# Kernel optimization log

Measured on AMD Instinct MI355X. Metric: run time of the kernel, lower is better.

Reference implementation:

```python
import jax, jax.numpy as jnp
import numpy as np

MASK_VAL = -2.0**32 + 1.0

def setup_inputs() -> dict:
    key = jax.random.key(0)
    ks = jax.random.split(key, 8)
    B, T, E = 4096, 200, 64
    H1, H2 = 64, 32
    return {
        "query": jax.random.normal(ks[0], (B, 1, E), dtype=jnp.float32),
        "keys": jax.random.normal(ks[1], (B, T, E), dtype=jnp.float32),
        "keys_len": jax.random.randint(ks[2], (B, 1), 0, T, dtype=jnp.int64),
        "W1": jax.random.normal(ks[3], (4 * E, H1), dtype=jnp.float32) * 0.05,
        "b1": jnp.zeros((H1,), dtype=jnp.float32),
        "W2": jax.random.normal(ks[4], (H1, H2), dtype=jnp.float32) * 0.05,
        "b2": jnp.zeros((H2,), dtype=jnp.float32),
        "W3": jax.random.normal(ks[5], (H2, 1), dtype=jnp.float32) * 0.05,
        "b3": jnp.zeros((1,), dtype=jnp.float32),
    }

def reference(query, keys, keys_len, W1, b1, W2, b2, W3, b3):
    B, T, E = keys.shape
    q = jnp.broadcast_to(query, (B, T, E))                      # (B,T,E)
    x = jnp.concatenate([q, keys, q - keys, q * keys], axis=-1)  # (B,T,4E)
    h = jax.nn.relu(jnp.einsum('bti,ih->bth', x, W1) + b1)       # (B,T,H1)
    h = jax.nn.relu(jnp.einsum('bth,ho->bto', h, W2) + b2)       # (B,T,H2)
    score = jnp.einsum('bto,oc->btc', h, W3) + b3                # (B,T,1)
    score = jnp.transpose(score, (0, 2, 1))                      # (B,1,T)
    mask = (jnp.arange(T)[None, :] < keys_len)[:, None, :]       # (B,1,T)
    scores = jnp.where(mask, score, jnp.float32(MASK_VAL))
    scores = jax.nn.softmax(scores, axis=-1)                     # weight_normalization=True
    return jnp.matmul(scores, keys)                              # (B,1,E)
```

## Files before the change

### kernel.cpp

```cpp
#include <hip/hip_runtime.h>

typedef __attribute__((ext_vector_type(8))) short short8_t;
typedef __attribute__((ext_vector_type(4))) float f32x4;

#define MASK_VAL (-4294967295.0f)
#define NEG_BIG  (-1e30f)

__device__ __forceinline__ short f2bf(float x) {
    unsigned u;
    __builtin_memcpy(&u, &x, 4);
    u += 0x7FFFu + ((u >> 16) & 1u);
    return (short)(u >> 16);
}
__device__ __forceinline__ float bf2f(short s) {
    unsigned u = ((unsigned)(unsigned short)s) << 16;
    float f;
    __builtin_memcpy(&f, &u, 4);
    return f;
}

__global__ void prep_fold(const float* __restrict__ W1, const float* __restrict__ W2,
                          void* __restrict__ ws)
{
    short* wkT = (short*)ws;
    short* wdT = wkT + 4096;
    short* w2T = wkT + 8192;
    float* wac = (float*)((char*)ws + 20480);
    const int tid = threadIdx.x;
    for (int idx = tid; idx < 4096; idx += 256) {
        int n = idx & 63, k = idx >> 6;
        float a  = W1[4096  + idx];
        float c  = W1[8192  + idx];
        float d  = W1[12288 + idx];
        wkT[n * 64 + k] = f2bf(a - c);
        wdT[n * 64 + k] = f2bf(d);
        wac[idx] = W1[idx] + c;
    }
    for (int idx = tid; idx < 2048; idx += 256) {
        int o = idx & 31, h = idx >> 5;
        w2T[o * 64 + h] = f2bf(W2[idx]);
    }
}

__global__ __launch_bounds__(256) void prep_cs(
    const float* __restrict__ query, const float* __restrict__ b1,
    void* __restrict__ ws, int B)
{
    const float* wac = (const float*)((const char*)ws + 20480);
    float* csAll     = (float*)((char*)ws + 36864);
    __shared__ float wacs[4096];
    __shared__ float qsb[16 * 64];
    __shared__ float b1s[64];
    const int tid = threadIdx.x;
    const int g0  = blockIdx.x * 16;
    for (int i = tid; i < 1024; i += 256)
        ((float4*)wacs)[i] = ((const float4*)wac)[i];
    {
        int nb = B - g0; if (nb > 16) nb = 16;
        for (int i = tid; i < nb * 16; i += 256)
            ((float4*)qsb)[i] = ((const float4*)(query + (size_t)g0 * 64))[i];
    }
    if (tid < 64) b1s[tid] = b1[tid];
    __syncthreads();
    for (int o = tid; o < 1024; o += 256) {
        int bb = o >> 6, h = o & 63;
        if (g0 + bb >= B) continue;
        float acc = b1s[h];
#pragma unroll 16
        for (int i = 0; i < 64; ++i)
            acc += qsb[bb * 64 + i] * wacs[i * 64 + h];
        csAll[(size_t)(g0 + bb) * 64 + h] = acc;
    }
}

__global__ __launch_bounds__(256, 2) void attn_main(
    const float* __restrict__ query,
    const float* __restrict__ keys,
    const int*   __restrict__ keys_len,
    const float* __restrict__ b2,
    const float* __restrict__ W3,
    const float* __restrict__ b3,
    const void*  __restrict__ ws,
    float* __restrict__ out,
    int B)
{
    constexpr int STR = 72;
    const short* wkT   = (const short*)ws;
    const short* wdT   = wkT + 4096;
    const short* w2T   = wkT + 8192;
    const float* csAll = (const float*)((const char*)ws + 36864);

    __shared__ short Bk[64 * STR];
    __shared__ short Bd[64 * STR];
    __shared__ short W2s[32 * STR];
    __shared__ short h1w[4][16 * STR];
    __shared__ float swv[4][16];

    const int tid  = threadIdx.x;
    const int lane = tid & 63;
    const int wid  = tid >> 6;
    const int col  = lane & 15;
    const int quad = lane >> 4;
    const int b    = blockIdx.x * 4 + wid;
    const bool act = (b < B);

    for (int c = tid; c < 512; c += 256) {
        int r = c >> 3, ch = (c & 7) * 8;
        *(short8_t*)&Bk[r * STR + ch] = *(const short8_t*)(wkT + r * 64 + ch);
        *(short8_t*)&Bd[r * STR + ch] = *(const short8_t*)(wdT + r * 64 + ch);
    }
    {
        int r = tid >> 3, ch = (tid & 7) * 8;
        *(short8_t*)&W2s[r * STR + ch] = *(const short8_t*)(w2T + r * 64 + ch);
    }

    const float* kb = nullptr;
    float4 n0, n1, n2, n3;
    float4 qv0, qv1, qv2, qv3;
    float cs0 = 0.f, cs1 = 0.f, cs2 = 0.f, cs3 = 0.f;
    float b2a = 0.f, b2b = 0.f, w3a = 0.f, w3b = 0.f, b3v = 0.f;
    if (act) {
        kb = keys + (size_t)b * 12800;
        {
            const float* kr = kb + col * 64 + quad * 8;
            n0 = *(const float4*)(kr);
            n1 = *(const float4*)(kr + 4);
            n2 = *(const float4*)(kr + 32);
            n3 = *(const float4*)(kr + 36);
        }
        const float* qb = query + (size_t)b * 64;
        qv0 = *(const float4*)(qb + quad * 8);
        qv1 = *(const float4*)(qb + quad * 8 + 4);
        qv2 = *(const float4*)(qb + 32 + quad * 8);
        qv3 = *(const float4*)(qb + 32 + quad * 8 + 4);
        const float* cb = csAll + (size_t)b * 64;
        cs0 = cb[col]; cs1 = cb[16 + col]; cs2 = cb[32 + col]; cs3 = cb[48 + col];
        b2a = b2[col];      b2b = b2[col + 16];
        w3a = W3[col];      w3b = W3[col + 16];
        b3v = b3[0];
    }
    __syncthreads();
    if (!act) return;

    const int len = keys_len[b];
    short* hw = h1w[wid];

    float m_run = NEG_BIG, l_run = 0.f;
    float accv[16];
#pragma unroll
    for (int i = 0; i < 16; ++i) accv[i] = 0.f;

    for (int jt = 0; jt < 13; ++jt) {
        float4 k0 = n0, k1 = n1, k2 = n2, k3 = n3;
        if (jt < 12) {
            int row = jt * 16 + 16 + col;
            row = row < 200 ? row : 199;
            const float* kr = kb + row * 64 + quad * 8;
            n0 = *(const float4*)(kr);
            n1 = *(const float4*)(kr + 4);
            n2 = *(const float4*)(kr + 32);
            n3 = *(const float4*)(kr + 36);
        }

        short8_t aK0, aK1, aQ0, aQ1;
        aK0[0] = f2bf(k0.x); aK0[1] = f2bf(k0.y); aK0[2] = f2bf(k0.z); aK0[3] = f2bf(k0.w);
        aK0[4] = f2bf(k1.x); aK0[5] = f2bf(k1.y); aK0[6] = f2bf(k1.z); aK0[7] = f2bf(k1.w);
        aK1[0] = f2bf(k2.x); aK1[1] = f2bf(k2.y); aK1[2] = f2bf(k2.z); aK1[3] = f2bf(k2.w);
        aK1[4] = f2bf(k3.x); aK1[5] = f2bf(k3.y); aK1[6] = f2bf(k3.z); aK1[7] = f2bf(k3.w);
        aQ0[0] = f2bf(k0.x * qv0.x); aQ0[1] = f2bf(k0.y * qv0.y);
        aQ0[2] = f2bf(k0.z * qv0.z); aQ0[3] = f2bf(k0.w * qv0.w);
        aQ0[4] = f2bf(k1.x * qv1.x); aQ0[5] = f2bf(k1.y * qv1.y);
        aQ0[6] = f2bf(k1.z * qv1.z); aQ0[7] = f2bf(k1.w * qv1.w);
        aQ1[0] = f2bf(k2.x * qv2.x); aQ1[1] = f2bf(k2.y * qv2.y);
        aQ1[2] = f2bf(k2.z * qv2.z); aQ1[3] = f2bf(k2.w * qv2.w);
        aQ1[4] = f2bf(k3.x * qv3.x); aQ1[5] = f2bf(k3.y * qv3.y);
        aQ1[6] = f2bf(k3.z * qv3.z); aQ1[7] = f2bf(k3.w * qv3.w);

        f32x4 acc[4] = {f32x4{0,0,0,0}, f32x4{0,0,0,0}, f32x4{0,0,0,0}, f32x4{0,0,0,0}};
#pragma unroll
        for (int nt = 0; nt < 4; ++nt) {
            const short* bp = &Bk[(nt * 16 + col) * STR + quad * 8];
            const short* dp = &Bd[(nt * 16 + col) * STR + quad * 8];
            acc[nt] = __builtin_amdgcn_mfma_f32_16x16x32_bf16(aK0, *(const short8_t*)bp,        acc[nt], 0, 0, 0);
            acc[nt] = __builtin_amdgcn_mfma_f32_16x16x32_bf16(aK1, *(const short8_t*)(bp + 32), acc[nt], 0, 0, 0);
            acc[nt] = __builtin_amdgcn_mfma_f32_16x16x32_bf16(aQ0, *(const short8_t*)dp,        acc[nt], 0, 0, 0);
            acc[nt] = __builtin_amdgcn_mfma_f32_16x16x32_bf16(aQ1, *(const short8_t*)(dp + 32), acc[nt], 0, 0, 0);
        }

        float csv[4] = {cs0, cs1, cs2, cs3};
#pragma unroll
        for (int nt = 0; nt < 4; ++nt) {
            float cadd = csv[nt];
#pragma unroll
            for (int r = 0; r < 4; ++r)
                hw[(quad * 4 + r) * STR + nt * 16 + col] = f2bf(fmaxf(acc[nt][r] + cadd, 0.f));
        }

        f32x4 acc2a = f32x4{0,0,0,0}, acc2b = f32x4{0,0,0,0};
#pragma unroll
        for (int ks = 0; ks < 2; ++ks) {
            short8_t a2 = *(const short8_t*)&hw[col * STR + ks * 32 + quad * 8];
            acc2a = __builtin_amdgcn_mfma_f32_16x16x32_bf16(
                a2, *(const short8_t*)&W2s[col * STR + ks * 32 + quad * 8], acc2a, 0, 0, 0);
            acc2b = __builtin_amdgcn_mfma_f32_16x16x32_bf16(
                a2, *(const short8_t*)&W2s[(16 + col) * STR + ks * 32 + quad * 8], acc2b, 0, 0, 0);
        }

#pragma unroll
        for (int r = 0; r < 4; ++r) {
            float v = fmaxf(acc2a[r] + b2a, 0.f) * w3a
                    + fmaxf(acc2b[r] + b2b, 0.f) * w3b;
            v += __shfl_xor(v, 1);
            v += __shfl_xor(v, 2);
            v += __shfl_xor(v, 4);
            v += __shfl_xor(v, 8);
            if (col == 0) swv[wid][quad * 4 + r] = v + b3v;
        }
        float sv = swv[wid][col];

        int  row  = jt * 16 + col;
        bool vrow = row < 200;
        sv = (row < len) ? sv : MASK_VAL;
        float svm = vrow ? sv : NEG_BIG;
        svm = fmaxf(svm, __shfl_xor(svm, 1));
        svm = fmaxf(svm, __shfl_xor(svm, 2));
        svm = fmaxf(svm, __shfl_xor(svm, 4));
        svm = fmaxf(svm, __shfl_xor(svm, 8));
        float m_new = fmaxf(m_run, svm);
        float p = vrow ? __expf(sv - m_new) : 0.f;
        float ps = p;
        ps += __shfl_xor(ps, 1);
        ps += __shfl_xor(ps, 2);
        ps += __shfl_xor(ps, 4);
        ps += __shfl_xor(ps, 8);
        if (m_new > m_run) {
            float scale = __expf(m_run - m_new);
            l_run *= scale;
#pragma unroll
            for (int i = 0; i < 16; ++i) accv[i] *= scale;
            m_run = m_new;
        }
        l_run += ps;
#pragma unroll
        for (int i = 0; i < 8; ++i) {
            accv[i]     += p * bf2f(aK0[i]);
            accv[8 + i] += p * bf2f(aK1[i]);
        }
    }

    float inv = 1.f / l_run;
#pragma unroll
    for (int i = 0; i < 16; ++i) {
        float v = accv[i];
        v += __shfl_xor(v, 1);
        v += __shfl_xor(v, 2);
        v += __shfl_xor(v, 4);
        v += __shfl_xor(v, 8);
        accv[i] = v * inv;
    }
    if (col == 0) {
        float* op = out + (size_t)b * 64;
        *(float4*)(op + quad * 8)          = make_float4(accv[0],  accv[1],  accv[2],  accv[3]);
        *(float4*)(op + quad * 8 + 4)      = make_float4(accv[4],  accv[5],  accv[6],  accv[7]);
        *(float4*)(op + 32 + quad * 8)     = make_float4(accv[8],  accv[9],  accv[10], accv[11]);
        *(float4*)(op + 32 + quad * 8 + 4) = make_float4(accv[12], accv[13], accv[14], accv[15]);
    }
}

extern "C" void kernel_launch(void* const* d_in, const int* in_sizes, int n_in,
                              void* d_out, int out_size, void* d_ws, size_t ws_size,
                              hipStream_t stream) {
    const float* query    = (const float*)d_in[0];
    const float* keys     = (const float*)d_in[1];
    const int*   keys_len = (const int*)d_in[2];
    const float* W1       = (const float*)d_in[3];
    const float* b1       = (const float*)d_in[4];
    const float* W2       = (const float*)d_in[5];
    const float* b2       = (const float*)d_in[6];
    const float* W3       = (const float*)d_in[7];
    const float* b3       = (const float*)d_in[8];
    float* out            = (float*)d_out;

    const int B = in_sizes[1] / 12800;

    prep_fold<<<dim3(1), dim3(256), 0, stream>>>(W1, W2, d_ws);
    prep_cs<<<dim3((B + 15) / 16), dim3(256), 0, stream>>>(query, b1, d_ws, B);
    attn_main<<<dim3((B + 3) / 4), dim3(256), 0, stream>>>(
        query, keys, keys_len, b2, W3, b3, d_ws, out, B);
}
```

Before: 327.8 us.

## Merge prep kernels, deepen key prefetch, transpose layer-2 MFMA to drop LDS score reduction

```diff
diff --git a/kernel.cpp b/kernel.cpp
--- a/kernel.cpp
+++ b/kernel.cpp
@@ -19,46 +19,44 @@
     return f;
 }
 
-__global__ void prep_fold(const float* __restrict__ W1, const float* __restrict__ W2,
-                          void* __restrict__ ws)
+__global__ __launch_bounds__(256) void prep_all(
+    const float* __restrict__ W1, const float* __restrict__ W2,
+    const float* __restrict__ query, const float* __restrict__ b1,
+    void* __restrict__ ws, int B)
 {
     short* wkT = (short*)ws;
     short* wdT = wkT + 4096;
     short* w2T = wkT + 8192;
-    float* wac = (float*)((char*)ws + 20480);
+    float* csAll = (float*)((char*)ws + 36864);
     const int tid = threadIdx.x;
-    for (int idx = tid; idx < 4096; idx += 256) {
-        int n = idx & 63, k = idx >> 6;
-        float a  = W1[4096  + idx];
-        float c  = W1[8192  + idx];
-        float d  = W1[12288 + idx];
-        wkT[n * 64 + k] = f2bf(a - c);
-        wdT[n * 64 + k] = f2bf(d);
-        wac[idx] = W1[idx] + c;
-    }
-    for (int idx = tid; idx < 2048; idx += 256) {
-        int o = idx & 31, h = idx >> 5;
-        w2T[o * 64 + h] = f2bf(W2[idx]);
-    }
-}
-
-__global__ __launch_bounds__(256) void prep_cs(
-    const float* __restrict__ query, const float* __restrict__ b1,
-    void* __restrict__ ws, int B)
-{
-    const float* wac = (const float*)((const char*)ws + 20480);
-    float* csAll     = (float*)((char*)ws + 36864);
+
+    if (blockIdx.x == 0) {
+        for (int idx = tid; idx < 4096; idx += 256) {
+            int n = idx & 63, k = idx >> 6;
+            float a  = W1[4096  + idx];
+            float c  = W1[8192  + idx];
+            float d  = W1[12288 + idx];
+            wkT[n * 64 + k] = f2bf(a - c);
+            wdT[n * 64 + k] = f2bf(d);
+        }
+        for (int idx = tid; idx < 2048; idx += 256) {
+            int o = idx & 31, h = idx >> 5;
+            w2T[o * 64 + h] = f2bf(W2[idx]);
+        }
+        return;
+    }
+
     __shared__ float wacs[4096];
     __shared__ float qsb[16 * 64];
     __shared__ float b1s[64];
-    const int tid = threadIdx.x;
-    const int g0  = blockIdx.x * 16;
-    for (int i = tid; i < 1024; i += 256)
-        ((float4*)wacs)[i] = ((const float4*)wac)[i];
+    const int g0 = (blockIdx.x - 1) * 16;
+    for (int idx = tid; idx < 4096; idx += 256)
+        wacs[idx] = W1[idx] + W1[8192 + idx];
     {
         int nb = B - g0; if (nb > 16) nb = 16;
-        for (int i = tid; i < nb * 16; i += 256)
-            ((float4*)qsb)[i] = ((const float4*)(query + (size_t)g0 * 64))[i];
+        if (nb > 0)
+            for (int i = tid; i < nb * 16; i += 256)
+                ((float4*)qsb)[i] = ((const float4*)(query + (size_t)g0 * 64))[i];
     }
     if (tid < 64) b1s[tid] = b1[tid];
     __syncthreads();
@@ -73,7 +71,7 @@
     }
 }
 
-__global__ __launch_bounds__(256, 2) void attn_main(
+__global__ __launch_bounds__(256, 3) void attn_main(
     const float* __restrict__ query,
     const float* __restrict__ keys,
     const int*   __restrict__ keys_len,
@@ -94,7 +92,6 @@
     __shared__ short Bd[64 * STR];
     __shared__ short W2s[32 * STR];
     __shared__ short h1w[4][16 * STR];
-    __shared__ float swv[4][16];
 
     const int tid  = threadIdx.x;
     const int lane = tid & 63;
@@ -115,18 +112,26 @@
     }
 
     const float* kb = nullptr;
-    float4 n0, n1, n2, n3;
+    float4 pA0, pA1, pA2, pA3;
+    float4 pB0, pB1, pB2, pB3;
     float4 qv0, qv1, qv2, qv3;
-    float cs0 = 0.f, cs1 = 0.f, cs2 = 0.f, cs3 = 0.f;
-    float b2a = 0.f, b2b = 0.f, w3a = 0.f, w3b = 0.f, b3v = 0.f;
+    float4 b2qa, b2qb, w3qa, w3qb;
+    float cs0 = 0.f, cs1 = 0.f, cs2 = 0.f, cs3 = 0.f, b3v = 0.f;
     if (act) {
         kb = keys + (size_t)b * 12800;
         {
             const float* kr = kb + col * 64 + quad * 8;
-            n0 = *(const float4*)(kr);
-            n1 = *(const float4*)(kr + 4);
-            n2 = *(const float4*)(kr + 32);
-            n3 = *(const float4*)(kr + 36);
+            pA0 = *(const float4*)(kr);
+            pA1 = *(const float4*)(kr + 4);
+            pA2 = *(const float4*)(kr + 32);
+            pA3 = *(const float4*)(kr + 36);
+        }
+        {
+            const float* kr = kb + (16 + col) * 64 + quad * 8;
+            pB0 = *(const float4*)(kr);
+            pB1 = *(const float4*)(kr + 4);
+            pB2 = *(const float4*)(kr + 32);
+            pB3 = *(const float4*)(kr + 36);
         }
         const float* qb = query + (size_t)b * 64;
         qv0 = *(const float4*)(qb + quad * 8);
@@ -135,9 +140,11 @@
         qv3 = *(const float4*)(qb + 32 + quad * 8 + 4);
         const float* cb = csAll + (size_t)b * 64;
         cs0 = cb[col]; cs1 = cb[16 + col]; cs2 = cb[32 + col]; cs3 = cb[48 + col];
-        b2a = b2[col];      b2b = b2[col + 16];
-        w3a = W3[col];      w3b = W3[col + 16];
-        b3v = b3[0];
+        b2qa = *(const float4*)(b2 + quad * 4);
+        b2qb = *(const float4*)(b2 + 16 + quad * 4);
+        w3qa = *(const float4*)(W3 + quad * 4);
+        w3qb = *(const float4*)(W3 + 16 + quad * 4);
+        b3v  = b3[0];
     }
     __syncthreads();
     if (!act) return;
@@ -150,18 +157,7 @@
 #pragma unroll
     for (int i = 0; i < 16; ++i) accv[i] = 0.f;
 
-    for (int jt = 0; jt < 13; ++jt) {
-        float4 k0 = n0, k1 = n1, k2 = n2, k3 = n3;
-        if (jt < 12) {
-            int row = jt * 16 + 16 + col;
-            row = row < 200 ? row : 199;
-            const float* kr = kb + row * 64 + quad * 8;
-            n0 = *(const float4*)(kr);
-            n1 = *(const float4*)(kr + 4);
-            n2 = *(const float4*)(kr + 32);
-            n3 = *(const float4*)(kr + 36);
-        }
-
+    auto tile = [&](int jt, float4 k0, float4 k1, float4 k2, float4 k3) {
         short8_t aK0, aK1, aQ0, aQ1;
         aK0[0] = f2bf(k0.x); aK0[1] = f2bf(k0.y); aK0[2] = f2bf(k0.z); aK0[3] = f2bf(k0.w);
         aK0[4] = f2bf(k1.x); aK0[5] = f2bf(k1.y); aK0[6] = f2bf(k1.z); aK0[7] = f2bf(k1.w);
@@ -199,24 +195,22 @@
         f32x4 acc2a = f32x4{0,0,0,0}, acc2b = f32x4{0,0,0,0};
 #pragma unroll
         for (int ks = 0; ks < 2; ++ks) {
-            short8_t a2 = *(const short8_t*)&hw[col * STR + ks * 32 + quad * 8];
+            short8_t h1f = *(const short8_t*)&hw[col * STR + ks * 32 + quad * 8];
             acc2a = __builtin_amdgcn_mfma_f32_16x16x32_bf16(
-                a2, *(const short8_t*)&W2s[col * STR + ks * 32 + quad * 8], acc2a, 0, 0, 0);
+                *(const short8_t*)&W2s[col * STR + ks * 32 + quad * 8],        h1f, acc2a, 0, 0, 0);
             acc2b = __builtin_amdgcn_mfma_f32_16x16x32_bf16(
-                a2, *(const short8_t*)&W2s[(16 + col) * STR + ks * 32 + quad * 8], acc2b, 0, 0, 0);
-        }
-
+                *(const short8_t*)&W2s[(16 + col) * STR + ks * 32 + quad * 8], h1f, acc2b, 0, 0, 0);
+        }
+
+        float sp = 0.f;
 #pragma unroll
         for (int r = 0; r < 4; ++r) {
-            float v = fmaxf(acc2a[r] + b2a, 0.f) * w3a
-                    + fmaxf(acc2b[r] + b2b, 0.f) * w3b;
-            v += __shfl_xor(v, 1);
-            v += __shfl_xor(v, 2);
-            v += __shfl_xor(v, 4);
-            v += __shfl_xor(v, 8);
-            if (col == 0) swv[wid][quad * 4 + r] = v + b3v;
-        }
-        float sv = swv[wid][col];
+            sp += fmaxf(acc2a[r] + b2qa[r], 0.f) * w3qa[r]
+                + fmaxf(acc2b[r] + b2qb[r], 0.f) * w3qb[r];
+        }
+        sp += __shfl_xor(sp, 16);
+        sp += __shfl_xor(sp, 32);
+        float sv = sp + b3v;
 
         int  row  = jt * 16 + col;
         bool vrow = row < 200;
@@ -246,7 +240,35 @@
             accv[i]     += p * bf2f(aK0[i]);
             accv[8 + i] += p * bf2f(aK1[i]);
         }
-    }
+    };
+
+#pragma unroll 1
+    for (int i = 0; i < 6; ++i) {
+        const int jt = i * 2;
+        float4 c0 = pA0, c1 = pA1, c2 = pA2, c3 = pA3;
+        {
+            int row = (jt + 2) * 16 + col;
+            row = row < 200 ? row : 199;
+            const float* kr = kb + row * 64 + quad * 8;
+            pA0 = *(const float4*)(kr);
+            pA1 = *(const float4*)(kr + 4);
+            pA2 = *(const float4*)(kr + 32);
+            pA3 = *(const float4*)(kr + 36);
+        }
+        tile(jt, c0, c1, c2, c3);
+        float4 d0 = pB0, d1 = pB1, d2 = pB2, d3 = pB3;
+        {
+            int row = (jt + 3) * 16 + col;
+            row = row < 200 ? row : 199;
+            const float* kr = kb + row * 64 + quad * 8;
+            pB0 = *(const float4*)(kr);
+            pB1 = *(const float4*)(kr + 4);
+            pB2 = *(const float4*)(kr + 32);
+            pB3 = *(const float4*)(kr + 36);
+        }
+        tile(jt + 1, d0, d1, d2, d3);
+    }
+    tile(12, pA0, pA1, pA2, pA3);
 
     float inv = 1.f / l_run;
 #pragma unroll
@@ -283,8 +305,7 @@
 
     const int B = in_sizes[1] / 12800;
 
-    prep_fold<<<dim3(1), dim3(256), 0, stream>>>(W1, W2, d_ws);
-    prep_cs<<<dim3((B + 15) / 16), dim3(256), 0, stream>>>(query, b1, d_ws, B);
+    prep_all<<<dim3(1 + (B + 15) / 16), dim3(256), 0, stream>>>(W1, W2, query, b1, d_ws, B);
     attn_main<<<dim3((B + 3) / 4), dim3(256), 0, stream>>>(
         query, keys, keys_len, b2, W3, b3, d_ws, out, B);
 }
```

Result: slower. 478.4 us (+45.9%).
